# Kernel tuning notes

Measured on AMD Instinct MI355X. Metric: run time of the kernel, lower is better.

## Reference

```python
import jax, jax.numpy as jnp
import numpy as np

INPUT_SIZE = 32
HIDDEN_SIZE = 128
N_HEAD = 8
NER_NUMS = 8
D = INPUT_SIZE * NER_NUMS  # 256, attention feature dim per head


def setup_inputs() -> dict:
    key = jax.random.key(0)
    ks = jax.random.split(key, 10)
    B, S = 8, 2048
    x = jax.random.normal(ks[0], (B, S, D), dtype=jnp.float32)
    bi_lstm_o = jax.random.normal(ks[1], (B, S, 2 * HIDDEN_SIZE), dtype=jnp.float32)
    # per-head linear params, stacked on leading head axis (nn.init.normal_ -> std 1)
    Qw = jax.random.normal(ks[2], (N_HEAD, 2 * HIDDEN_SIZE, D), dtype=jnp.float32)
    Qb = jax.random.normal(ks[3], (N_HEAD, D), dtype=jnp.float32)
    Kw = jax.random.normal(ks[4], (N_HEAD, D, D), dtype=jnp.float32)
    Kb = jax.random.normal(ks[5], (N_HEAD, D), dtype=jnp.float32)
    Vw = jax.random.normal(ks[6], (N_HEAD, D, D), dtype=jnp.float32)
    Vb = jax.random.normal(ks[7], (N_HEAD, D), dtype=jnp.float32)
    Cw = jax.random.normal(ks[8], (N_HEAD * D, NER_NUMS), dtype=jnp.float32)
    Cb = jax.random.normal(ks[9], (NER_NUMS,), dtype=jnp.float32)
    return {"x": x, "bi_lstm_o": bi_lstm_o, "Qw": Qw, "Qb": Qb, "Kw": Kw,
            "Kb": Kb, "Vw": Vw, "Vb": Vb, "Cw": Cw, "Cb": Cb}


def reference(x, bi_lstm_o, Qw, Qb, Kw, Kb, Vw, Vb, Cw, Cb):
    # q from bi_lstm_o, k/v from x; all heads batched on axis h
    q = jnp.einsum('bsf,hfd->hbsd', bi_lstm_o, Qw) + Qb[:, None, None, :]
    k = jnp.einsum('bsf,hfd->hbsd', x, Kw) + Kb[:, None, None, :]
    v = jnp.einsum('bsf,hfd->hbsd', x, Vw) + Vb[:, None, None, :]
    scale = 1.0 / jnp.sqrt(jnp.float32(D))
    scores = jnp.einsum('hbsd,hbtd->hbst', q, k) * scale  # [H,B,S,S]
    attn = jax.nn.softmax(scores, axis=-1)
    o = jnp.einsum('hbst,hbtd->hbsd', attn, v)  # [H,B,S,D]
    B, S = x.shape[0], x.shape[1]
    concat = jnp.transpose(o, (1, 2, 0, 3)).reshape(B, S, N_HEAD * D)  # head order matches torch.cat
    return concat @ Cw + Cb
```

## Files before the change

### kernel.cpp

```cpp
#include <hip/hip_runtime.h>

#define H_ 8
#define B_ 8
#define S_ 2048
#define D_ 256

#define KSTRIDE 264
#define VSTRIDE 40
#define QTSTRIDE 136

typedef __attribute__((ext_vector_type(8))) _Float16 half8;
typedef __attribute__((ext_vector_type(4))) _Float16 half4v;
typedef __attribute__((ext_vector_type(2))) _Float16 half2v;
typedef __attribute__((ext_vector_type(4))) float f32x4;

__device__ inline void split8(const float* __restrict__ p, half8& hv, half8& lv) {
  float4 a = *(const float4*)p, b = *(const float4*)(p + 4);
  hv[0] = (_Float16)a.x; hv[1] = (_Float16)a.y; hv[2] = (_Float16)a.z; hv[3] = (_Float16)a.w;
  hv[4] = (_Float16)b.x; hv[5] = (_Float16)b.y; hv[6] = (_Float16)b.z; hv[7] = (_Float16)b.w;
  lv[0] = (_Float16)(a.x - (float)hv[0]); lv[1] = (_Float16)(a.y - (float)hv[1]);
  lv[2] = (_Float16)(a.z - (float)hv[2]); lv[3] = (_Float16)(a.w - (float)hv[3]);
  lv[4] = (_Float16)(b.x - (float)hv[4]); lv[5] = (_Float16)(b.y - (float)hv[5]);
  lv[6] = (_Float16)(b.z - (float)hv[6]); lv[7] = (_Float16)(b.w - (float)hv[7]);
}

__global__ void split_w_kernel(const float* __restrict__ W,
                               _Float16* __restrict__ thi, _Float16* __restrict__ tlo) {
  __shared__ float t[64][65];
  const int h = blockIdx.z, f0 = blockIdx.x * 64, d0 = blockIdx.y * 64;
  const int col = threadIdx.x & 63, rg = threadIdx.x >> 6;
#pragma unroll
  for (int it = 0; it < 16; ++it) {
    int f = rg * 16 + it;
    t[f][col] = W[((size_t)h * 256 + f0 + f) * 256 + d0 + col];
  }
  __syncthreads();
#pragma unroll
  for (int it = 0; it < 16; ++it) {
    int d = rg * 16 + it;
    float v = t[col][d];
    _Float16 hv = (_Float16)v;
    size_t idx = ((size_t)h * 256 + d0 + d) * 256 + f0 + col;
    thi[idx] = hv;
    tlo[idx] = (_Float16)(v - (float)hv);
  }
}

__global__ void out_init_kernel(float* __restrict__ out, const float* __restrict__ Cb) {
  int i = blockIdx.x * blockDim.x + threadIdx.x;
  if (i < B_ * S_ * 8) out[i] = Cb[i & 7];
}

template <int VMODE>
__global__ __launch_bounds__(256, 2) void proj_kernel(
    const float* __restrict__ A,
    const _Float16* __restrict__ Whi, const _Float16* __restrict__ Wlo,
    const float* __restrict__ bias, float oscale, int h0,
    _Float16* __restrict__ Ohi, _Float16* __restrict__ Olo) {
  constexpr bool TMULT = (VMODE != 1);
  __shared__ _Float16 a_hi[128 * VSTRIDE] __attribute__((aligned(16)));
  __shared__ _Float16 b_hi[128 * VSTRIDE] __attribute__((aligned(16)));
  __shared__ _Float16 a_lo[TMULT ? 128 * VSTRIDE : 8] __attribute__((aligned(16)));
  __shared__ _Float16 b_lo[TMULT ? 128 * VSTRIDE : 8] __attribute__((aligned(16)));
  const int tid = threadIdx.x;
  const int w = tid >> 6, lane = tid & 63;
  const int quad = lane >> 4, l15 = lane & 15;
  const int hb = blockIdx.z, h = h0 + (hb >> 3), b = hb & 7;
  const int s0 = blockIdx.x * 128, d0 = blockIdx.y * 128;
  const int wr = w >> 1, wc = w & 1;
  const f32x4 fz = {0.f, 0.f, 0.f, 0.f};
  f32x4 acc[4][4];
#pragma unroll
  for (int i = 0; i < 4; ++i)
#pragma unroll
    for (int j = 0; j < 4; ++j) acc[i][j] = fz;
  const size_t arow0 = (size_t)b * S_ + s0;
  const size_t wrow0 = (size_t)h * 256 + d0;
  for (int kk = 0; kk < 8; ++kk) {
    const int f0 = kk * 32;
    __syncthreads();
#pragma unroll
    for (int i = 0; i < 2; ++i) {
      int cc = i * 256 + tid;
      int r = cc >> 2, ch = (cc & 3) * 8;
      half8 hv, lv;
      split8(A + (arow0 + r) * 256 + f0 + ch, hv, lv);
      *(half8*)&a_hi[r * VSTRIDE + ch] = hv;
      size_t woff = (wrow0 + r) * 256 + f0 + ch;
      *(half8*)&b_hi[r * VSTRIDE + ch] = *(const half8*)(Whi + woff);
      if (TMULT) {
        *(half8*)&a_lo[r * VSTRIDE + ch] = lv;
        *(half8*)&b_lo[r * VSTRIDE + ch] = *(const half8*)(Wlo + woff);
      }
    }
    __syncthreads();
    half8 afh[4], afl[4], bfh[4], bfl[4];
#pragma unroll
    for (int t = 0; t < 4; ++t) {
      int ar = wr * 64 + t * 16 + l15;
      afh[t] = *(const half8*)&a_hi[ar * VSTRIDE + quad * 8];
      int br = wc * 64 + t * 16 + l15;
      bfh[t] = *(const half8*)&b_hi[br * VSTRIDE + quad * 8];
      if (TMULT) {
        afl[t] = *(const half8*)&a_lo[ar * VSTRIDE + quad * 8];
        bfl[t] = *(const half8*)&b_lo[br * VSTRIDE + quad * 8];
      }
    }
#pragma unroll
    for (int rf = 0; rf < 4; ++rf)
#pragma unroll
      for (int cf = 0; cf < 4; ++cf) {
        acc[rf][cf] = __builtin_amdgcn_mfma_f32_16x16x32_f16(afh[rf], bfh[cf], acc[rf][cf], 0, 0, 0);
        if (TMULT) {
          acc[rf][cf] = __builtin_amdgcn_mfma_f32_16x16x32_f16(afh[rf], bfl[cf], acc[rf][cf], 0, 0, 0);
          acc[rf][cf] = __builtin_amdgcn_mfma_f32_16x16x32_f16(afl[rf], bfh[cf], acc[rf][cf], 0, 0, 0);
        }
      }
  }
#pragma unroll
  for (int rf = 0; rf < 4; ++rf) {
#pragma unroll
    for (int cf = 0; cf < 4; ++cf) {
      const int d = d0 + wc * 64 + cf * 16 + l15;
      const float bv = bias[h * 256 + d];
      if (VMODE != 1) {
#pragma unroll
        for (int r = 0; r < 4; ++r) {
          const int s = s0 + wr * 64 + rf * 16 + quad * 4 + r;
          float val = (acc[rf][cf][r] + bv) * oscale;
          _Float16 hvv = (_Float16)val;
          size_t idx = ((size_t)hb * S_ + s) * 256 + d;
          Ohi[idx] = hvv;
          if (VMODE == 0) Olo[idx] = (_Float16)(val - (float)hvv);
        }
      } else {
        half4v pack;
#pragma unroll
        for (int r = 0; r < 4; ++r) pack[r] = (_Float16)((acc[rf][cf][r] + bv) * oscale);
        size_t idx = ((size_t)hb * 256 + d) * S_ + s0 + wr * 64 + rf * 16 + quad * 4;
        *(half4v*)(Ohi + idx) = pack;
      }
    }
  }
}

__global__ __launch_bounds__(256, 2) void flash_kernel(
    const float* __restrict__ bo,
    const _Float16* __restrict__ qwhi, const _Float16* __restrict__ qwlo,
    const float* __restrict__ qbias,
    const _Float16* __restrict__ khi,
    const _Float16* __restrict__ vt, const float* __restrict__ Cw,
    float* __restrict__ out, int h0) {
  __shared__ _Float16 khi_s[32 * KSTRIDE] __attribute__((aligned(16)));
  __shared__ _Float16 vt_s[256 * VSTRIDE] __attribute__((aligned(16)));
  __shared__ _Float16 p_s[4][16 * VSTRIDE] __attribute__((aligned(16)));
  __shared__ _Float16 wbuf[256 * VSTRIDE] __attribute__((aligned(16)));
  const int tid = threadIdx.x, w = tid >> 6, lane = tid & 63;
  const int quad = lane >> 4, l15 = lane & 15;
  const int nheads = gridDim.y >> 3;
  const int bid = blockIdx.x + gridDim.x * blockIdx.y;
  const int hloc = bid % nheads;
  const int rr = bid / nheads;
  const int b = rr & 7;
  const int qblk = rr >> 3;
  const int h = h0 + hloc;
  const int hb = hloc * 8 + b;
  const int qbase = qblk * 64;
  _Float16* psf = &p_s[0][0];

  const f32x4 fz = {0.f, 0.f, 0.f, 0.f};
  f32x4 qacc[16];
#pragma unroll
  for (int df = 0; df < 16; ++df) qacc[df] = fz;
  for (int kk = 0; kk < 8; ++kk) {
    __syncthreads();
#pragma unroll
    for (int i = 0; i < 4; ++i) {
      int c = i * 256 + tid;
      int dr = c >> 2, ch = (c & 3) * 8;
      size_t woff = ((size_t)h * 256 + dr) * 256 + kk * 32 + ch;
      *(half8*)&vt_s[dr * VSTRIDE + ch] = *(const half8*)(qwhi + woff);
      *(half8*)&wbuf[dr * VSTRIDE + ch] = *(const half8*)(qwlo + woff);
    }
    {
      int rrow = tid >> 2, ch = (tid & 3) * 8;
      half8 hv, lv;
      split8(bo + ((size_t)b * S_ + qbase + rrow) * 256 + kk * 32 + ch, hv, lv);
      *(half8*)&khi_s[rrow * VSTRIDE + ch] = hv;
      *(half8*)&psf[rrow * VSTRIDE + ch] = lv;
    }
    __syncthreads();
    half8 bh = *(const half8*)&khi_s[(w * 16 + l15) * VSTRIDE + quad * 8];
    half8 bl = *(const half8*)&psf[(w * 16 + l15) * VSTRIDE + quad * 8];
#pragma unroll
    for (int df = 0; df < 16; ++df) {
      half8 awh = *(const half8*)&vt_s[(df * 16 + l15) * VSTRIDE + quad * 8];
      half8 awl = *(const half8*)&wbuf[(df * 16 + l15) * VSTRIDE + quad * 8];
      qacc[df] = __builtin_amdgcn_mfma_f32_16x16x32_f16(awh, bh, qacc[df], 0, 0, 0);
      qacc[df] = __builtin_amdgcn_mfma_f32_16x16x32_f16(awl, bh, qacc[df], 0, 0, 0);
      qacc[df] = __builtin_amdgcn_mfma_f32_16x16x32_f16(awh, bl, qacc[df], 0, 0, 0);
    }
  }
  half8 qfh[8], qfl[8];
#pragma unroll
  for (int ph = 0; ph < 4; ++ph) {
    const bool lo = ph >= 2;
    const int dh = (ph & 1) * 8;
    __syncthreads();
#pragma unroll
    for (int dfi = 0; dfi < 8; ++dfi) {
      int df = dh + dfi;
#pragma unroll
      for (int rp = 0; rp < 2; ++rp) {
        half2v hw;
#pragma unroll
        for (int rr2 = 0; rr2 < 2; ++rr2) {
          int r = rp * 2 + rr2;
          float bv = qbias[h * 256 + df * 16 + quad * 4 + r];
          float val = (qacc[df][r] + bv) * 0.0625f;
          _Float16 hv = (_Float16)val;
          hw[rr2] = lo ? (_Float16)(val - (float)hv) : hv;
        }
        *(half2v*)&vt_s[(w * 16 + l15) * QTSTRIDE + dfi * 16 + quad * 4 + rp * 2] = hw;
      }
    }
    __syncthreads();
#pragma unroll
    for (int k2 = 0; k2 < 4; ++k2) {
      half8 v = *(const half8*)&vt_s[(w * 16 + l15) * QTSTRIDE + k2 * 32 + quad * 8];
      if (lo) qfl[(ph & 1) * 4 + k2] = v;
      else    qfh[(ph & 1) * 4 + k2] = v;
    }
  }

  f32x4 o_acc[16];
#pragma unroll
  for (int df = 0; df < 16; ++df) o_acc[df] = fz;
  float m_r = -3.0e38f, l_r = 0.f;

  for (int kt = 0; kt < 64; ++kt) {
    __syncthreads();
    {
      size_t kbase = ((size_t)hb * S_ + kt * 32) * 256;
#pragma unroll
      for (int i = 0; i < 4; ++i) {
        int cc = i * 256 + tid;
        int kr = cc >> 5, kch = (cc & 31) * 8;
        *(half8*)&khi_s[kr * KSTRIDE + kch] = *(const half8*)(khi + kbase + kr * 256 + kch);
        int vd = cc >> 2, vch = (cc & 3) * 8;
        size_t voff = ((size_t)hb * 256 + vd) * S_ + kt * 32 + vch;
        *(half8*)&vt_s[vd * VSTRIDE + vch] = *(const half8*)(vt + voff);
      }
    }
    __syncthreads();
    f32x4 sc0 = fz, sc1 = fz;
#pragma unroll
    for (int ks = 0; ks < 8; ++ks) {
      half8 bh0 = *(const half8*)&khi_s[(0 * 16 + l15) * KSTRIDE + ks * 32 + quad * 8];
      sc0 = __builtin_amdgcn_mfma_f32_16x16x32_f16(bh0, qfh[ks], sc0, 0, 0, 0);
      sc0 = __builtin_amdgcn_mfma_f32_16x16x32_f16(bh0, qfl[ks], sc0, 0, 0, 0);
      half8 bh1 = *(const half8*)&khi_s[(1 * 16 + l15) * KSTRIDE + ks * 32 + quad * 8];
      sc1 = __builtin_amdgcn_mfma_f32_16x16x32_f16(bh1, qfh[ks], sc1, 0, 0, 0);
      sc1 = __builtin_amdgcn_mfma_f32_16x16x32_f16(bh1, qfl[ks], sc1, 0, 0, 0);
    }
    float v = fmaxf(fmaxf(fmaxf(sc0[0], sc0[1]), fmaxf(sc0[2], sc0[3])),
                    fmaxf(fmaxf(sc1[0], sc1[1]), fmaxf(sc1[2], sc1[3])));
    v = fmaxf(v, __shfl_xor(v, 16));
    v = fmaxf(v, __shfl_xor(v, 32));
    const float mn = fmaxf(m_r, v);
    const float al = __expf(m_r - mn);
    m_r = mn;
    float p0[4], p1[4], s = 0.f;
#pragma unroll
    for (int r = 0; r < 4; ++r) {
      p0[r] = __expf(sc0[r] - mn);
      p1[r] = __expf(sc1[r] - mn);
      s += p0[r] + p1[r];
    }
    s += __shfl_xor(s, 16);
    s += __shfl_xor(s, 32);
    l_r = l_r * al + s;
    {
      _Float16* pb = &p_s[w][l15 * VSTRIDE + quad * 4];
      half2v w0 = {(_Float16)p0[0], (_Float16)p0[1]};
      half2v w1 = {(_Float16)p0[2], (_Float16)p0[3]};
      half2v w2 = {(_Float16)p1[0], (_Float16)p1[1]};
      half2v w3 = {(_Float16)p1[2], (_Float16)p1[3]};
      *(half2v*)(pb) = w0;
      *(half2v*)(pb + 2) = w1;
      *(half2v*)(pb + 16) = w2;
      *(half2v*)(pb + 18) = w3;
    }
    float al_r[4];
#pragma unroll
    for (int r = 0; r < 4; ++r) al_r[r] = __shfl(al, quad * 4 + r);
#pragma unroll
    for (int df = 0; df < 16; ++df)
#pragma unroll
      for (int r = 0; r < 4; ++r) o_acc[df][r] *= al_r[r];
    __syncthreads();
    half8 pf = *(const half8*)&p_s[w][l15 * VSTRIDE + quad * 8];
#pragma unroll
    for (int df = 0; df < 16; ++df) {
      half8 vf = *(const half8*)&vt_s[(df * 16 + l15) * VSTRIDE + quad * 8];
      o_acc[df] = __builtin_amdgcn_mfma_f32_16x16x32_f16(pf, vf, o_acc[df], 0, 0, 0);
    }
  }
  float rcl[4];
#pragma unroll
  for (int r = 0; r < 4; ++r) rcl[r] = 1.0f / __shfl(l_r, quad * 4 + r);
  float part[32];
#pragma unroll
  for (int i = 0; i < 32; ++i) part[i] = 0.f;
#pragma unroll
  for (int df = 0; df < 16; ++df) {
    const float4* cwv = (const float4*)(Cw + ((size_t)h * 256 + df * 16 + l15) * 8);
    float4 c0 = cwv[0], c1 = cwv[1];
#pragma unroll
    for (int r = 0; r < 4; ++r) {
      float ov = o_acc[df][r] * rcl[r];
      part[r * 8 + 0] += ov * c0.x;
      part[r * 8 + 1] += ov * c0.y;
      part[r * 8 + 2] += ov * c0.z;
      part[r * 8 + 3] += ov * c0.w;
      part[r * 8 + 4] += ov * c1.x;
      part[r * 8 + 5] += ov * c1.y;
      part[r * 8 + 6] += ov * c1.z;
      part[r * 8 + 7] += ov * c1.w;
    }
  }
#pragma unroll
  for (int i = 0; i < 32; ++i) {
    float v = part[i];
    v += __shfl_xor(v, 1);
    v += __shfl_xor(v, 2);
    v += __shfl_xor(v, 4);
    v += __shfl_xor(v, 8);
    part[i] = v;
  }
  if (l15 == 0) {
#pragma unroll
    for (int r = 0; r < 4; ++r) {
      int s = qbase + w * 16 + quad * 4 + r;
#pragma unroll
      for (int j = 0; j < 8; ++j)
        atomicAdd(&out[((size_t)b * S_ + s) * 8 + j], part[r * 8 + j]);
    }
  }
}

extern "C" void kernel_launch(void* const* d_in, const int* in_sizes, int n_in,
                              void* d_out, int out_size, void* d_ws, size_t ws_size,
                              hipStream_t stream) {
  const float* x  = (const float*)d_in[0];
  const float* bo = (const float*)d_in[1];
  const float* Qw = (const float*)d_in[2];
  const float* Qb = (const float*)d_in[3];
  const float* Kw = (const float*)d_in[4];
  const float* Kb = (const float*)d_in[5];
  const float* Vw = (const float*)d_in[6];
  const float* Vb = (const float*)d_in[7];
  const float* Cw = (const float*)d_in[8];
  const float* Cb = (const float*)d_in[9];
  float* out = (float*)d_out;

  const size_t NW  = (size_t)H_ * 256 * 256;
  const size_t NHB = (size_t)B_ * S_ * 256;
  const size_t ALN = 256;
  auto pad = [](size_t b) { return (b + 255) & ~(size_t)255; };

  int HC = 8;
  while (HC > 1) {
    size_t need = 6 * pad(NW * 2) + 2 * pad((size_t)HC * NHB * 2) + ALN;
    if (need <= ws_size) break;
    HC >>= 1;
  }

  char* base = (char*)d_ws;
  size_t off = 0;
  auto carve = [&](size_t nelem) -> _Float16* {
    _Float16* p = (_Float16*)(base + off);
    off += pad(nelem * 2);
    return p;
  };
  _Float16* qwt_hi = carve(NW); _Float16* qwt_lo = carve(NW);
  _Float16* kwt_hi = carve(NW); _Float16* kwt_lo = carve(NW);
  _Float16* vwt_hi = carve(NW); _Float16* vwt_lo = carve(NW);
  const size_t NC = (size_t)HC * NHB;
  _Float16* k_hi = carve(NC);
  _Float16* v_t  = carve(NC);

  dim3 wg(4, 4, 8);
  split_w_kernel<<<wg, 256, 0, stream>>>(Qw, qwt_hi, qwt_lo);
  split_w_kernel<<<wg, 256, 0, stream>>>(Kw, kwt_hi, kwt_lo);
  split_w_kernel<<<wg, 256, 0, stream>>>(Vw, vwt_hi, vwt_lo);
  out_init_kernel<<<(B_ * S_ * 8) / 256, 256, 0, stream>>>(out, Cb);

  for (int h0 = 0; h0 < H_; h0 += HC) {
    dim3 pg(16, 2, HC * 8);
    proj_kernel<2><<<pg, 256, 0, stream>>>(x, kwt_hi, kwt_lo, Kb, 1.0f, h0, k_hi, nullptr);
    proj_kernel<1><<<pg, 256, 0, stream>>>(x, vwt_hi, vwt_lo, Vb, 1.0f, h0, v_t, nullptr);
    dim3 fg(32, HC * 8);
    flash_kernel<<<fg, 256, 0, stream>>>(bo, qwt_hi, qwt_lo, Qb, k_hi, v_t, Cw, out, h0);
  }
}
```

Measured before the change: 896.8 us.

## Double flash block to 512 threads covering 128 queries with aliased shared memory

The flash kernel now runs 8 waves per block over 128 query rows instead of 4 waves over 64, so each K/V tile staged in shared memory is reused by twice as many queries. Shared buffers are merged into one array whose regions are aliased between the Q-projection phase and the attention loop, which keeps LDS use per block small enough for several blocks per CU. The grid is halved to match. Launch bounds change to 512 threads with a minimum of 4 blocks, which tightens the register budget. Given the large accumulator arrays, that could cause spilling.

Result: slower. 1.375 ms (+53.3%).

```diff
diff --git a/kernel.cpp b/kernel.cpp
--- a/kernel.cpp
+++ b/kernel.cpp
@@ -144,17 +144,22 @@
   }
 }
 
-__global__ __launch_bounds__(256, 2) void flash_kernel(
+__global__ __launch_bounds__(512, 4) void flash_kernel(
     const float* __restrict__ bo,
     const _Float16* __restrict__ qwhi, const _Float16* __restrict__ qwlo,
     const float* __restrict__ qbias,
     const _Float16* __restrict__ khi,
     const _Float16* __restrict__ vt, const float* __restrict__ Cw,
     float* __restrict__ out, int h0) {
-  __shared__ _Float16 khi_s[32 * KSTRIDE] __attribute__((aligned(16)));
-  __shared__ _Float16 vt_s[256 * VSTRIDE] __attribute__((aligned(16)));
-  __shared__ _Float16 p_s[4][16 * VSTRIDE] __attribute__((aligned(16)));
-  __shared__ _Float16 wbuf[256 * VSTRIDE] __attribute__((aligned(16)));
+  __shared__ _Float16 smem[30720] __attribute__((aligned(16)));
+  _Float16* khi_s = smem;
+  _Float16* vt_s  = smem + 8448;
+  _Float16* p_s   = smem + 18688;
+  _Float16* qw_hi = smem;
+  _Float16* qw_lo = smem + 10240;
+  _Float16* bo_hi = smem + 20480;
+  _Float16* bo_lo = smem + 25600;
+  _Float16* qtb   = smem;
   const int tid = threadIdx.x, w = tid >> 6, lane = tid & 63;
   const int quad = lane >> 4, l15 = lane & 15;
   const int nheads = gridDim.y >> 3;
@@ -165,8 +170,7 @@
   const int qblk = rr >> 3;
   const int h = h0 + hloc;
   const int hb = hloc * 8 + b;
-  const int qbase = qblk * 64;
-  _Float16* psf = &p_s[0][0];
+  const int qbase = qblk * 128;
 
   const f32x4 fz = {0.f, 0.f, 0.f, 0.f};
   f32x4 qacc[16];
@@ -175,27 +179,27 @@
   for (int kk = 0; kk < 8; ++kk) {
     __syncthreads();
 #pragma unroll
-    for (int i = 0; i < 4; ++i) {
-      int c = i * 256 + tid;
+    for (int i = 0; i < 2; ++i) {
+      int c = i * 512 + tid;
       int dr = c >> 2, ch = (c & 3) * 8;
       size_t woff = ((size_t)h * 256 + dr) * 256 + kk * 32 + ch;
-      *(half8*)&vt_s[dr * VSTRIDE + ch] = *(const half8*)(qwhi + woff);
-      *(half8*)&wbuf[dr * VSTRIDE + ch] = *(const half8*)(qwlo + woff);
+      *(half8*)&qw_hi[dr * VSTRIDE + ch] = *(const half8*)(qwhi + woff);
+      *(half8*)&qw_lo[dr * VSTRIDE + ch] = *(const half8*)(qwlo + woff);
     }
     {
       int rrow = tid >> 2, ch = (tid & 3) * 8;
       half8 hv, lv;
       split8(bo + ((size_t)b * S_ + qbase + rrow) * 256 + kk * 32 + ch, hv, lv);
-      *(half8*)&khi_s[rrow * VSTRIDE + ch] = hv;
-      *(half8*)&psf[rrow * VSTRIDE + ch] = lv;
-    }
-    __syncthreads();
-    half8 bh = *(const half8*)&khi_s[(w * 16 + l15) * VSTRIDE + quad * 8];
-    half8 bl = *(const half8*)&psf[(w * 16 + l15) * VSTRIDE + quad * 8];
+      *(half8*)&bo_hi[rrow * VSTRIDE + ch] = hv;
+      *(half8*)&bo_lo[rrow * VSTRIDE + ch] = lv;
+    }
+    __syncthreads();
+    half8 bh = *(const half8*)&bo_hi[(w * 16 + l15) * VSTRIDE + quad * 8];
+    half8 bl = *(const half8*)&bo_lo[(w * 16 + l15) * VSTRIDE + quad * 8];
 #pragma unroll
     for (int df = 0; df < 16; ++df) {
-      half8 awh = *(const half8*)&vt_s[(df * 16 + l15) * VSTRIDE + quad * 8];
-      half8 awl = *(const half8*)&wbuf[(df * 16 + l15) * VSTRIDE + quad * 8];
+      half8 awh = *(const half8*)&qw_hi[(df * 16 + l15) * VSTRIDE + quad * 8];
+      half8 awl = *(const half8*)&qw_lo[(df * 16 + l15) * VSTRIDE + quad * 8];
       qacc[df] = __builtin_amdgcn_mfma_f32_16x16x32_f16(awh, bh, qacc[df], 0, 0, 0);
       qacc[df] = __builtin_amdgcn_mfma_f32_16x16x32_f16(awl, bh, qacc[df], 0, 0, 0);
       qacc[df] = __builtin_amdgcn_mfma_f32_16x16x32_f16(awh, bl, qacc[df], 0, 0, 0);
@@ -204,12 +208,12 @@
   half8 qfh[8], qfl[8];
 #pragma unroll
   for (int ph = 0; ph < 4; ++ph) {
-    const bool lo = ph >= 2;
-    const int dh = (ph & 1) * 8;
+    const int dh = ph >> 1;
+    const bool lo = ph & 1;
     __syncthreads();
 #pragma unroll
     for (int dfi = 0; dfi < 8; ++dfi) {
-      int df = dh + dfi;
+      int df = dh * 8 + dfi;
 #pragma unroll
       for (int rp = 0; rp < 2; ++rp) {
         half2v hw;
@@ -221,15 +225,15 @@
           _Float16 hv = (_Float16)val;
           hw[rr2] = lo ? (_Float16)(val - (float)hv) : hv;
         }
-        *(half2v*)&vt_s[(w * 16 + l15) * QTSTRIDE + dfi * 16 + quad * 4 + rp * 2] = hw;
+        *(half2v*)&qtb[(w * 16 + l15) * QTSTRIDE + dfi * 16 + quad * 4 + rp * 2] = hw;
       }
     }
     __syncthreads();
 #pragma unroll
     for (int k2 = 0; k2 < 4; ++k2) {
-      half8 v = *(const half8*)&vt_s[(w * 16 + l15) * QTSTRIDE + k2 * 32 + quad * 8];
-      if (lo) qfl[(ph & 1) * 4 + k2] = v;
-      else    qfh[(ph & 1) * 4 + k2] = v;
+      half8 v = *(const half8*)&qtb[(w * 16 + l15) * QTSTRIDE + k2 * 32 + quad * 8];
+      if (lo) qfl[dh * 4 + k2] = v;
+      else    qfh[dh * 4 + k2] = v;
     }
   }
 
@@ -237,14 +241,15 @@
 #pragma unroll
   for (int df = 0; df < 16; ++df) o_acc[df] = fz;
   float m_r = -3.0e38f, l_r = 0.f;
+  _Float16* psw = p_s + w * (16 * VSTRIDE);
 
   for (int kt = 0; kt < 64; ++kt) {
     __syncthreads();
     {
       size_t kbase = ((size_t)hb * S_ + kt * 32) * 256;
 #pragma unroll
-      for (int i = 0; i < 4; ++i) {
-        int cc = i * 256 + tid;
+      for (int i = 0; i < 2; ++i) {
+        int cc = i * 512 + tid;
         int kr = cc >> 5, kch = (cc & 31) * 8;
         *(half8*)&khi_s[kr * KSTRIDE + kch] = *(const half8*)(khi + kbase + kr * 256 + kch);
         int vd = cc >> 2, vch = (cc & 3) * 8;
@@ -281,7 +286,7 @@
     s += __shfl_xor(s, 32);
     l_r = l_r * al + s;
     {
-      _Float16* pb = &p_s[w][l15 * VSTRIDE + quad * 4];
+      _Float16* pb = &psw[l15 * VSTRIDE + quad * 4];
       half2v w0 = {(_Float16)p0[0], (_Float16)p0[1]};
       half2v w1 = {(_Float16)p0[2], (_Float16)p0[3]};
       half2v w2 = {(_Float16)p1[0], (_Float16)p1[1]};
@@ -299,7 +304,7 @@
 #pragma unroll
       for (int r = 0; r < 4; ++r) o_acc[df][r] *= al_r[r];
     __syncthreads();
-    half8 pf = *(const half8*)&p_s[w][l15 * VSTRIDE + quad * 8];
+    half8 pf = *(const half8*)&psw[l15 * VSTRIDE + quad * 8];
 #pragma unroll
     for (int df = 0; df < 16; ++df) {
       half8 vf = *(const half8*)&vt_s[(df * 16 + l15) * VSTRIDE + quad * 8];
@@ -400,7 +405,7 @@
     dim3 pg(16, 2, HC * 8);
     proj_kernel<2><<<pg, 256, 0, stream>>>(x, kwt_hi, kwt_lo, Kb, 1.0f, h0, k_hi, nullptr);
     proj_kernel<1><<<pg, 256, 0, stream>>>(x, vwt_hi, vwt_lo, Vb, 1.0f, h0, v_t, nullptr);
-    dim3 fg(32, HC * 8);
-    flash_kernel<<<fg, 256, 0, stream>>>(bo, qwt_hi, qwt_lo, Qb, k_hi, v_t, Cw, out, h0);
-  }
-}
+    dim3 fg(16, HC * 8);
+    flash_kernel<<<fg, 512, 0, stream>>>(bo, qwt_hi, qwt_lo, Qb, k_hi, v_t, Cw, out, h0);
+  }
+}
```
